# Optimization experiments

Hardware: AMD Instinct MI355X
Metric: run time of the kernel (lower is better)

## Reference

```python
import jax, jax.numpy as jnp
import numpy as np

N = 50000   # nodes (= batch_size = num_e)
D = 256     # d_dim = n_hidden
E = 320000  # edges (first half 'in' direction, second half 'out'/inverse)
R = 400     # relation types (incl. inverses)


def setup_inputs() -> dict:
    key = jax.random.key(0)
    ks = jax.random.split(key, 12)
    s = 0.05  # weight scale so tanh stays in linear-ish range
    w = lambda k, shp: jax.random.normal(k, shp, jnp.float32) * s
    return {
        "emb": jax.random.normal(ks[0], (N, D), jnp.float32),
        "edge_index": jax.random.randint(ks[1], (2, E), 0, N),
        "edge_type": jax.random.randint(ks[2], (E,), 0, R),
        "rel1": w(ks[3], (R, D)),
        "W_in1": w(ks[4], (D, D)),
        "W_out1": w(ks[5], (D, D)),
        "W_loop1": w(ks[6], (D, D)),
        "b1": jnp.zeros((D,), jnp.float32),
        "rel2": w(ks[7], (R, D)),
        "W_in2": w(ks[8], (D, D)),
        "W_out2": w(ks[9], (D, D)),
        "W_loop2": w(ks[10], (D, D)),
        "b2": jnp.zeros((D,), jnp.float32),
        "res": jnp.array([0.1], jnp.float32),
        "mu_w": w(ks[11], (D, D)),
        "mu_b": jnp.zeros((D,), jnp.float32),
        "num_nodes": N,
    }


def _mgcn_conv(x, edge_index, edge_type, rel, W_in, W_out, W_loop, b, n):
    """Relational conv: gather -> compose with relation emb -> direction-split
    linear transform -> degree-normalized scatter-add -> self-loop -> tanh."""
    src, dst = edge_index[0], edge_index[1]
    e = edge_index.shape[1]
    half = e // 2
    m = x[src] * rel[edge_type]                                   # [E, D] compose ('mult')
    m = jnp.concatenate([m[:half] @ W_in, m[half:] @ W_out], 0)    # direction-specific transform
    deg = jax.ops.segment_sum(jnp.ones((e,), x.dtype), dst, num_segments=n)
    norm = 1.0 / jnp.maximum(deg, 1.0)                             # 1/in-degree
    agg = jax.ops.segment_sum(m * norm[dst][:, None], dst, num_segments=n)
    return jnp.tanh(agg + x @ W_loop + b)


def reference(emb, edge_index, edge_type,
              rel1, W_in1, W_out1, W_loop1, b1,
              rel2, W_in2, W_out2, W_loop2, b2,
              res, mu_w, mu_b, num_nodes):
    # forward_base with p.res=True, core_layer=2, dropout in eval mode (identity)
    h = emb + res * _mgcn_conv(emb, edge_index, edge_type, rel1, W_in1, W_out1, W_loop1, b1, num_nodes)
    h = h + res * _mgcn_conv(h, edge_index, edge_type, rel2, W_in2, W_out2, W_loop2, b2, num_nodes)
    # drift head f(t, y) = mu(forward_base(y))
    return h @ mu_w + mu_b
```

## Files before the change

kernel.cpp:

```cpp
#include <hip/hip_runtime.h>
#include <hip/hip_bf16.h>
#include <cstdint>
#include <cstddef>


typedef short bf16x8 __attribute__((ext_vector_type(8)));
typedef float f32x4  __attribute__((ext_vector_type(4)));

__device__ __forceinline__ float b2f(unsigned short u) {
    union { unsigned u32; float f; } c; c.u32 = ((unsigned)u) << 16; return c.f;
}
__device__ __forceinline__ unsigned short f2b(float f) {
    union { float f; unsigned u; } c; c.f = f;
    unsigned r = c.u + 0x7FFFu + ((c.u >> 16) & 1u);
    return (unsigned short)(r >> 16);
}
__device__ __forceinline__ float ftanh(float x) {
    float e = __expf(2.0f * x);
    return 1.0f - __fdividef(2.0f, e + 1.0f);
}

__device__ __forceinline__ unsigned char f2e4m3(float f) {
    unsigned u = __float_as_uint(f);
    unsigned s = (u >> 24) & 0x80u;
    unsigned a = u & 0x7fffffffu;
    if (a >= 0x43e00000u) return (unsigned char)(s | 0x7eu);
    if (a < 0x3c800000u) {
        float m = __uint_as_float(a) * 512.0f;
        int q = (int)rintf(m);
        if (q == 8) return (unsigned char)(s | 0x08u);
        return (unsigned char)(s | (unsigned)q);
    }
    unsigned m = a & 0x7fffffu;
    unsigned e = a >> 23;
    unsigned r = m + 0x7ffffu + ((m >> 20) & 1u);
    if (r >= 0x800000u) { e += 1; r -= 0x800000u; }
    if (e > 127u + 8u) return (unsigned char)(s | 0x7eu);
    return (unsigned char)(s | ((e - 127u + 7u) << 3) | (r >> 20));
}


__global__ void k_hist(const int* __restrict__ dst, int* __restrict__ cnt, int E) {
    int i = blockIdx.x * blockDim.x + threadIdx.x;
    if (i < E) atomicAdd(&cnt[dst[i]], 1);
}

__global__ void k_norm(const int* __restrict__ cnt, float* __restrict__ norm, int N) {
    int i = blockIdx.x * blockDim.x + threadIdx.x;
    if (i < N) norm[i] = 1.0f / fmaxf((float)cnt[i], 1.0f);
}

__global__ void k_scan1(const int* __restrict__ cnt, int* __restrict__ part,
                        int* __restrict__ bsum, int N) {
    __shared__ int s[256];
    int i = blockIdx.x * 256 + threadIdx.x;
    int v = (i < N) ? cnt[i] : 0;
    s[threadIdx.x] = v; __syncthreads();
    #pragma unroll
    for (int o = 1; o < 256; o <<= 1) {
        int t = (threadIdx.x >= o) ? s[threadIdx.x - o] : 0;
        __syncthreads();
        s[threadIdx.x] += t;
        __syncthreads();
    }
    if (i < N) part[i] = s[threadIdx.x] - v;
    if (threadIdx.x == 255) bsum[blockIdx.x] = s[255];
}

__global__ void k_scan2(int* __restrict__ bsum, int nb) {
    __shared__ int s[256];
    int v = (threadIdx.x < nb) ? bsum[threadIdx.x] : 0;
    s[threadIdx.x] = v; __syncthreads();
    #pragma unroll
    for (int o = 1; o < 256; o <<= 1) {
        int t = (threadIdx.x >= o) ? s[threadIdx.x - o] : 0;
        __syncthreads();
        s[threadIdx.x] += t;
        __syncthreads();
    }
    if (threadIdx.x < nb) bsum[threadIdx.x] = s[threadIdx.x] - v;
}

__global__ void k_scan3(const int* __restrict__ part, const int* __restrict__ bsum,
                        int* __restrict__ rowptr, int* __restrict__ cursor, int N, int E) {
    int i = blockIdx.x * 256 + threadIdx.x;
    if (i < N) {
        int r = part[i] + bsum[blockIdx.x];
        rowptr[i] = r; cursor[i] = r;
    }
    if (i == 0) rowptr[N] = E;
}

__global__ void k_scatter(const int* __restrict__ src, const int* __restrict__ dst,
                          const int* __restrict__ et, int* __restrict__ cursor,
                          unsigned* __restrict__ erec, int E, int halfE) {
    int e = blockIdx.x * blockDim.x + threadIdx.x;
    if (e < E) {
        int d = dst[e];
        int pos = atomicAdd(&cursor[d], 1);
        unsigned rec = (unsigned)src[e] | ((unsigned)et[e] << 16)
                     | ((e >= halfE) ? 0x80000000u : 0u);
        erec[pos] = rec;
    }
}


__global__ void k_cvt3(const float* __restrict__ s0, unsigned short* __restrict__ d0, long n0,
                       const float* __restrict__ s1, unsigned short* __restrict__ d1, long n1,
                       const float* __restrict__ s2, unsigned short* __restrict__ d2, long n2) {
    long i = (long)blockIdx.x * blockDim.x + threadIdx.x;
    const float* s; unsigned short* d; long j = i;
    if (j < n0) { s = s0; d = d0; }
    else {
        j -= n0;
        if (j < n1) { s = s1; d = d1; }
        else { j -= n1; if (j >= n2) return; s = s2; d = d2; }
    }
    float4 v = ((const float4*)s)[j];
    ushort4 o;
    o.x = f2b(v.x); o.y = f2b(v.y); o.z = f2b(v.z); o.w = f2b(v.w);
    ((ushort4*)d)[j] = o;
}

__global__ void k_wfrag3(const float* __restrict__ w0, const float* __restrict__ w1,
                         const float* __restrict__ w2, unsigned short* __restrict__ out) {
    int o = blockIdx.x * 256 + threadIdx.x;
    int mi = o >> 16;
    int r  = o & 65535;
    const float* W = (mi == 0) ? w0 : (mi == 1) ? w1 : w2;
    int j  = r & 7;
    int l  = (r >> 3) & 63;
    int nn = (r >> 9) & 15;
    int kg = r >> 13;
    int k = kg * 32 + (l >> 4) * 8 + j;
    int n = nn * 16 + (l & 15);
    out[o] = f2b(W[k * 256 + n]);
}

__global__ void k_wfrag8(const float* __restrict__ w0, const float* __restrict__ w1,
                         const float* __restrict__ w2, const float* __restrict__ w3,
                         unsigned char* __restrict__ out) {
    int o = (blockIdx.x * 256 + threadIdx.x) * 4;
    int mi = o >> 16;
    int r  = o & 65535;
    const float* W = (mi == 0) ? w0 : (mi == 1) ? w1 : (mi == 2) ? w2 : w3;
    int j0 = r & 7;
    int l  = (r >> 3) & 63;
    int nn = (r >> 9) & 15;
    int kg = r >> 13;
    int n  = nn * 16 + (l & 15);
    int kb = kg * 32 + (l >> 4) * 8 + j0;
    unsigned b0 = f2e4m3(W[(kb + 0) * 256 + n]);
    unsigned b1 = f2e4m3(W[(kb + 1) * 256 + n]);
    unsigned b2 = f2e4m3(W[(kb + 2) * 256 + n]);
    unsigned b3 = f2e4m3(W[(kb + 3) * 256 + n]);
    *(unsigned*)(out + o) = b0 | (b1 << 8) | (b2 << 16) | (b3 << 24);
}


__global__ __launch_bounds__(256)
void k_agg(const unsigned short* __restrict__ xb, const unsigned short* __restrict__ relb,
           const int* __restrict__ rowptr, const unsigned* __restrict__ erec,
           const float* __restrict__ norm,
           unsigned char* __restrict__ sIn8, unsigned char* __restrict__ sOut8,
           int N, int D)
{
    const int w = threadIdx.x >> 6, l = threadIdx.x & 63;
    const int v = blockIdx.x * 4 + w;
    if (v >= N) return;
    const int rs = rowptr[v], re = rowptr[v + 1];
    const float nm = norm[v];

    float ai0 = 0, ai1 = 0, ai2 = 0, ai3 = 0;
    float ao0 = 0, ao1 = 0, ao2 = 0, ao3 = 0;

    unsigned c0 = (rs     < re) ? erec[rs]     : 0u;
    unsigned c1 = (rs + 1 < re) ? erec[rs + 1] : 0u;
    unsigned c2 = (rs + 2 < re) ? erec[rs + 2] : 0u;
    unsigned c3 = (rs + 3 < re) ? erec[rs + 3] : 0u;
    int i = rs;
    while (i + 4 <= re) {
        unsigned m0 = (i + 4 < re) ? erec[i + 4] : 0u;
        unsigned m1 = (i + 5 < re) ? erec[i + 5] : 0u;
        unsigned m2 = (i + 6 < re) ? erec[i + 6] : 0u;
        unsigned m3 = (i + 7 < re) ? erec[i + 7] : 0u;
        ushort4 x0 = *(const ushort4*)(xb   + (size_t)(c0 & 0xffff) * D + l * 4);
        ushort4 r0 = *(const ushort4*)(relb + (size_t)((c0 >> 16) & 0x7fff) * D + l * 4);
        ushort4 x1 = *(const ushort4*)(xb   + (size_t)(c1 & 0xffff) * D + l * 4);
        ushort4 r1 = *(const ushort4*)(relb + (size_t)((c1 >> 16) & 0x7fff) * D + l * 4);
        ushort4 x2 = *(const ushort4*)(xb   + (size_t)(c2 & 0xffff) * D + l * 4);
        ushort4 r2 = *(const ushort4*)(relb + (size_t)((c2 >> 16) & 0x7fff) * D + l * 4);
        ushort4 x3 = *(const ushort4*)(xb   + (size_t)(c3 & 0xffff) * D + l * 4);
        ushort4 r3 = *(const ushort4*)(relb + (size_t)((c3 >> 16) & 0x7fff) * D + l * 4);
        float p0, p1, p2, p3;
        p0 = b2f(x0.x)*b2f(r0.x); p1 = b2f(x0.y)*b2f(r0.y);
        p2 = b2f(x0.z)*b2f(r0.z); p3 = b2f(x0.w)*b2f(r0.w);
        if (c0 >> 31) { ao0 += p0; ao1 += p1; ao2 += p2; ao3 += p3; }
        else          { ai0 += p0; ai1 += p1; ai2 += p2; ai3 += p3; }
        p0 = b2f(x1.x)*b2f(r1.x); p1 = b2f(x1.y)*b2f(r1.y);
        p2 = b2f(x1.z)*b2f(r1.z); p3 = b2f(x1.w)*b2f(r1.w);
        if (c1 >> 31) { ao0 += p0; ao1 += p1; ao2 += p2; ao3 += p3; }
        else          { ai0 += p0; ai1 += p1; ai2 += p2; ai3 += p3; }
        p0 = b2f(x2.x)*b2f(r2.x); p1 = b2f(x2.y)*b2f(r2.y);
        p2 = b2f(x2.z)*b2f(r2.z); p3 = b2f(x2.w)*b2f(r2.w);
        if (c2 >> 31) { ao0 += p0; ao1 += p1; ao2 += p2; ao3 += p3; }
        else          { ai0 += p0; ai1 += p1; ai2 += p2; ai3 += p3; }
        p0 = b2f(x3.x)*b2f(r3.x); p1 = b2f(x3.y)*b2f(r3.y);
        p2 = b2f(x3.z)*b2f(r3.z); p3 = b2f(x3.w)*b2f(r3.w);
        if (c3 >> 31) { ao0 += p0; ao1 += p1; ao2 += p2; ao3 += p3; }
        else          { ai0 += p0; ai1 += p1; ai2 += p2; ai3 += p3; }
        c0 = m0; c1 = m1; c2 = m2; c3 = m3; i += 4;
    }
    #pragma unroll
    for (int j = 0; j < 3; ++j) {
        if (i + j < re) {
            unsigned cur = (j == 0) ? c0 : (j == 1) ? c1 : c2;
            ushort4 x0 = *(const ushort4*)(xb   + (size_t)(cur & 0xffff) * D + l * 4);
            ushort4 r0 = *(const ushort4*)(relb + (size_t)((cur >> 16) & 0x7fff) * D + l * 4);
            float p0 = b2f(x0.x)*b2f(r0.x), p1 = b2f(x0.y)*b2f(r0.y);
            float p2 = b2f(x0.z)*b2f(r0.z), p3 = b2f(x0.w)*b2f(r0.w);
            if (cur >> 31) { ao0 += p0; ao1 += p1; ao2 += p2; ao3 += p3; }
            else           { ai0 += p0; ai1 += p1; ai2 += p2; ai3 += p3; }
        }
    }

    unsigned pi = (unsigned)f2e4m3(ai0 * nm)        | ((unsigned)f2e4m3(ai1 * nm) << 8)
                | ((unsigned)f2e4m3(ai2 * nm) << 16) | ((unsigned)f2e4m3(ai3 * nm) << 24);
    unsigned po = (unsigned)f2e4m3(ao0 * nm)        | ((unsigned)f2e4m3(ao1 * nm) << 8)
                | ((unsigned)f2e4m3(ao2 * nm) << 16) | ((unsigned)f2e4m3(ao3 * nm) << 24);
    *(unsigned*)(sIn8  + (size_t)v * 256 + l * 4) = pi;
    *(unsigned*)(sOut8 + (size_t)v * 256 + l * 4) = po;
}


#define FB  do { asm volatile("s_waitcnt lgkmcnt(0)" ::: "memory");             \
                 __builtin_amdgcn_sched_barrier(0);                             \
                 __builtin_amdgcn_s_barrier();                                  \
                 __builtin_amdgcn_sched_barrier(0); } while (0)

#define WRX(AtN, R0, R1) do { *(uint4*)(&(AtN)[wo0]) = R0;                      \
                              *(uint4*)(&(AtN)[wo1]) = R1; } while (0)
#define WR8(AtN, R0)     do { *(uint4*)(((char*)(AtN)) + wf8b) = R0; } while (0)
#define LDX(R0, R1, CB)  do { R0 = *(const uint4*)(a0 + g0 + (CB)*64);          \
                              R1 = *(const uint4*)(a0 + g1 + (CB)*64); } while (0)
#define LD8(R0, SRC, CB) do { R0 = *(const uint4*)((SRC) + gf8 + (CB)*64); } while (0)

#define PBX(Bn, CB)                                                             \
  do { _Pragma("unroll")                                                        \
       for (int kk_ = 0; kk_ < 2; ++kk_) {                                      \
         _Pragma("unroll")                                                      \
         for (int n_ = 0; n_ < 4; ++n_)                                         \
           Bn[kk_*4+n_] = *(const bf16x8*)(WfL +                                \
               ((((CB)*2+kk_)*16 + (w*4+n_))*64 + l)*8);                        \
       } } while (0)

#define PB8(Bn, TBL, CB)                                                        \
  do { _Pragma("unroll")                                                        \
       for (int kk_ = 0; kk_ < 2; ++kk_) {                                      \
         _Pragma("unroll")                                                      \
         for (int n_ = 0; n_ < 4; ++n_)                                         \
           Bn[kk_*4+n_] = *(const long long*)((TBL) +                           \
               ((((CB)*2+kk_)*16 + (w*4+n_))*64 + l)*8);                        \
       } } while (0)

#define MMX(AtC, Bc)                                                            \
  do { _Pragma("unroll")                                                        \
       for (int kk_ = 0; kk_ < 2; ++kk_) {                                      \
         bf16x8 a_[4];                                                          \
         _Pragma("unroll")                                                      \
         for (int m_ = 0; m_ < 4; ++m_) {                                       \
           int rm_ = 16*m_ + lr; int ch_ = (kk_*4+lq) ^ (rm_ & 7);              \
           a_[m_] = *(const bf16x8*)(&(AtC)[rm_*64 + ch_*8]);                   \
         }                                                                      \
         _Pragma("unroll")                                                      \
         for (int m_ = 0; m_ < 4; ++m_) {                                       \
           _Pragma("unroll")                                                    \
           for (int n_ = 0; n_ < 4; ++n_)                                       \
             acc[m_][n_] = __builtin_amdgcn_mfma_f32_16x16x32_bf16(             \
                 a_[m_], Bc[kk_*4+n_], acc[m_][n_], 0, 0, 0);                   \
         } } } while (0)

#define MM8(AtC, Bc)                                                            \
  do { const char* A8_ = (const char*)(AtC);                                    \
       _Pragma("unroll")                                                        \
       for (int kk_ = 0; kk_ < 2; ++kk_) {                                      \
         long long a_[4];                                                       \
         _Pragma("unroll")                                                      \
         for (int m_ = 0; m_ < 4; ++m_) {                                       \
           int rm_ = 16*m_ + lr; int ch_ = (kk_*4+lq) ^ (rm_ & 6);              \
           a_[m_] = *(const long long*)(A8_ + rm_*64 + ch_*8);                  \
         }                                                                      \
         _Pragma("unroll")                                                      \
         for (int m_ = 0; m_ < 4; ++m_) {                                       \
           _Pragma("unroll")                                                    \
           for (int n_ = 0; n_ < 4; ++n_)                                       \
             acc[m_][n_] = __builtin_amdgcn_mfma_f32_16x16x32_fp8_fp8(          \
                 a_[m_], Bc[kk_*4+n_], acc[m_][n_], 0, 0, 0);                   \
         } } } while (0)

template <bool HEAD>
__global__ __launch_bounds__(256, 2)
void k_gemm(const unsigned short* __restrict__ a0,
            const unsigned char*  __restrict__ s8i,
            const unsigned char*  __restrict__ s8o,
            const unsigned short* __restrict__ WfL,
            const unsigned char*  __restrict__ W8I,
            const unsigned char*  __restrict__ W8O,
            const float* __restrict__ bias,
            const float* __restrict__ resPtr,
            const unsigned short* __restrict__ WfMu,
            const float* __restrict__ mub,
            float* __restrict__ outF,
            unsigned short* __restrict__ outB,
            int N, int D)
{
    __shared__ unsigned short lds[HEAD ? 16384 : 8192];
    unsigned short* At0 = lds;
    unsigned short* At1 = lds + 4096;

    const int t = threadIdx.x;
    const int rBase = blockIdx.x * 64;

    const int w  = t >> 6;
    const int l  = t & 63;
    const int lr = l & 15;
    const int lq = l >> 4;

    const int rS0 = t >> 3;
    const int rS1 = rS0 + 32;
    const int cS  = t & 7;
    const int wo0 = rS0 * 64 + ((cS ^ (rS0 & 7)) * 8);
    const int wo1 = rS1 * 64 + ((cS ^ (rS1 & 7)) * 8);
    const size_t g0 = (size_t)min(rBase + rS0, N - 1) * 256 + cS * 8;
    const size_t g1 = (size_t)min(rBase + rS1, N - 1) * 256 + cS * 8;

    const int rf  = t >> 2;
    const int qf  = t & 3;
    const int wf8b = rf * 64 + (((2 * qf) ^ (rf & 6)) * 8);
    const size_t gf8 = (size_t)min(rBase + rf, N - 1) * 256 + qf * 16;

    f32x4 acc[4][4] = {};
    uint4 Ra0, Ra1, Rb0, Rb1, Rc0, Rc1;
    bf16x8 Bb0[8], Bb1[8];
    long long B8a[8], B8b[8];

    LDX(Ra0, Ra1, 0);
    LDX(Rb0, Rb1, 1);
    LDX(Rc0, Rc1, 2);
    PBX(Bb0, 0);
    WRX(At0, Ra0, Ra1);
    FB;

     WRX(At1, Rb0, Rb1); PBX(Bb1, 1);      MMX(At0, Bb0); LDX(Ra0, Ra1, 3); FB;
     WRX(At0, Rc0, Rc1); PBX(Bb0, 2);      MMX(At1, Bb1); LD8(Rb0, s8i, 0); FB;
     WRX(At1, Ra0, Ra1); PBX(Bb1, 3);      MMX(At0, Bb0); LD8(Rc0, s8i, 1); FB;
     WR8(At0, Rb0);      PB8(B8a, W8I, 0); MMX(At1, Bb1); LD8(Ra0, s8i, 2); FB;
     WR8(At1, Rc0);      PB8(B8b, W8I, 1); MM8(At0, B8a); LD8(Rb0, s8i, 3); FB;
     WR8(At0, Ra0);      PB8(B8a, W8I, 2); MM8(At1, B8b); LD8(Rc0, s8o, 0); FB;
     WR8(At1, Rb0);      PB8(B8b, W8I, 3); MM8(At0, B8a); LD8(Ra0, s8o, 1); FB;
     WR8(At0, Rc0);      PB8(B8a, W8O, 0); MM8(At1, B8b); LD8(Rb0, s8o, 2); FB;
     WR8(At1, Ra0);      PB8(B8b, W8O, 1); MM8(At0, B8a); LD8(Rc0, s8o, 3); FB;
     WR8(At0, Rb0);      PB8(B8a, W8O, 2); MM8(At1, B8b); FB;
    WR8(At1, Rc0);      PB8(B8b, W8O, 3); MM8(At0, B8a); FB;
                                          MM8(At1, B8b); FB;

    const int rb4 = lq * 4;
    const float resv = resPtr[0];

    if (!HEAD) {
        unsigned short* C = lds;
        #pragma unroll
        for (int half = 0; half < 2; ++half) {
            if ((w >> 1) == half) {
                #pragma unroll
                for (int m = 0; m < 4; ++m) {
                    #pragma unroll
                    for (int i = 0; i < 4; ++i) {
                        int r6 = 16 * m + rb4 + i;
                        #pragma unroll
                        for (int n = 0; n < 4; ++n) {
                            int cH = (w & 1) * 64 + lr + 16 * n;
                            float v = acc[m][n][i] + bias[half * 128 + cH];
                            C[r6 * 128 + cH] = f2b(resv * ftanh(v));
                        }
                    }
                }
            }
            __syncthreads();
            #pragma unroll
            for (int ii = 0; ii < 4; ++ii) {
                int g   = ii * 256 + t;
                int r   = g >> 4;
                int cc  = g & 15;
                int row = rBase + r;
                if (row < N) {
                    bf16x8 sv = *(const bf16x8*)(&C[r * 128 + cc * 8]);
                    const unsigned short* ar = a0 + (size_t)row * D + half * 128 + cc * 8;
                    uint4 av = *(const uint4*)ar;
                    unsigned aw[4] = { av.x, av.y, av.z, av.w };
                    unsigned ow[4];
                    #pragma unroll
                    for (int p = 0; p < 4; ++p) {
                        float h0 = b2f((unsigned short)(aw[p] & 0xffff)) + b2f((unsigned short)sv[2 * p]);
                        float h1 = b2f((unsigned short)(aw[p] >> 16))    + b2f((unsigned short)sv[2 * p + 1]);
                        ow[p] = (unsigned)f2b(h0) | ((unsigned)f2b(h1) << 16);
                    }
                    *(uint4*)(outB + (size_t)row * D + half * 128 + cc * 8) =
                        make_uint4(ow[0], ow[1], ow[2], ow[3]);
                }
            }
            __syncthreads();
        }
    } else {
        #pragma unroll
        for (int m = 0; m < 4; ++m) {
            #pragma unroll
            for (int i = 0; i < 4; ++i) {
                int row = rBase + 16 * m + rb4 + i;
                if (row < N) {
                    size_t base = (size_t)row * D + w * 64 + lr;
                    int r6 = 16 * m + rb4 + i;
                    #pragma unroll
                    for (int n = 0; n < 4; ++n) {
                        int   c = w * 64 + lr + 16 * n;
                        float v = acc[m][n][i] + bias[c];
                        float h = b2f(a0[base + 16 * n]) + resv * ftanh(v);
                        lds[r6 * 256 + (c ^ ((r6 & 7) << 3))] = f2b(h);
                    }
                }
            }
        }
        __syncthreads();
        #pragma unroll
        for (int m = 0; m < 4; ++m) {
            #pragma unroll
            for (int n = 0; n < 4; ++n)
                acc[m][n] = (f32x4){0.f, 0.f, 0.f, 0.f};
        }

        #pragma unroll
        for (int s2 = 0; s2 < 4; ++s2) {
            #pragma unroll
            for (int kk = 0; kk < 2; ++kk) {
                const int kg = s2 * 2 + kk;
                bf16x8 a_[4], b_[4];
                #pragma unroll
                for (int m = 0; m < 4; ++m) {
                    int rm = 16 * m + lr;
                    int ch = (s2 * 8 + kk * 4 + lq) ^ (rm & 7);
                    a_[m] = *(const bf16x8*)(&lds[rm * 256 + ch * 8]);
                }
                #pragma unroll
                for (int n = 0; n < 4; ++n)
                    b_[n] = *(const bf16x8*)(WfMu + (((kg * 16 + (w * 4 + n)) * 64 + l) * 8));
                #pragma unroll
                for (int m = 0; m < 4; ++m) {
                    #pragma unroll
                    for (int n = 0; n < 4; ++n)
                        acc[m][n] = __builtin_amdgcn_mfma_f32_16x16x32_bf16(a_[m], b_[n], acc[m][n], 0, 0, 0);
                }
            }
        }

        __syncthreads();
        float* Cf = (float*)lds;
        #pragma unroll
        for (int half = 0; half < 2; ++half) {
            if ((w >> 1) == half) {
                #pragma unroll
                for (int m = 0; m < 4; ++m) {
                    #pragma unroll
                    for (int i = 0; i < 4; ++i) {
                        int r6 = 16 * m + rb4 + i;
                        #pragma unroll
                        for (int n = 0; n < 4; ++n) {
                            int cH = (w & 1) * 64 + lr + 16 * n;
                            Cf[r6 * 128 + cH] = acc[m][n][i] + mub[half * 128 + cH];
                        }
                    }
                }
            }
            __syncthreads();
            #pragma unroll
            for (int ii = 0; ii < 8; ++ii) {
                int g   = ii * 256 + t;
                int r   = g >> 5;
                int cc  = g & 31;
                int row = rBase + r;
                if (row < N) {
                    *(float4*)(outF + (size_t)row * D + half * 128 + cc * 4) =
                        *(const float4*)(&Cf[r * 128 + cc * 4]);
                }
            }
            __syncthreads();
        }
    }
}


extern "C" void kernel_launch(void* const* d_in, const int* in_sizes, int n_in,
                              void* d_out, int out_size, void* d_ws, size_t ws_size,
                              hipStream_t stream)
{
    const float* emb  = (const float*)d_in[0];
    const int*   ei   = (const int*)  d_in[1];
    const int*   et   = (const int*)  d_in[2];
    const float* rel1 = (const float*)d_in[3];
    const float* Wi1  = (const float*)d_in[4];
    const float* Wo1  = (const float*)d_in[5];
    const float* Wl1  = (const float*)d_in[6];
    const float* b1   = (const float*)d_in[7];
    const float* rel2 = (const float*)d_in[8];
    const float* Wi2  = (const float*)d_in[9];
    const float* Wo2  = (const float*)d_in[10];
    const float* Wl2  = (const float*)d_in[11];
    const float* b2   = (const float*)d_in[12];
    const float* res  = (const float*)d_in[13];
    const float* muw  = (const float*)d_in[14];
    const float* mub  = (const float*)d_in[15];

    const int D = in_sizes[7];
    const int N = in_sizes[0] / D;
    const int E = in_sizes[2];
    const int R = in_sizes[3] / D;
    const int halfE = E / 2;
    const int* srcA = ei;
    const int* dstA = ei + E;
    const size_t DD = (size_t)D * D;

    char* ws = (char*)d_ws;
    size_t off = 0;
    auto alloc = [&](size_t bytes) -> char* {
        char* p = ws + off; off += (bytes + 255) & ~(size_t)255; return p;
    };
    const int nb1 = (N + 255) / 256;

    float*          norm   = (float*)          alloc((size_t)N * 4);
    int*            cnt    = (int*)            alloc((size_t)N * 4);
    int*            rowptr = (int*)            alloc((size_t)(N + 1) * 4);
    int*            cursor = (int*)            alloc((size_t)N * 4);
    int*            part   = (int*)            alloc((size_t)N * 4);
    int*            bsum   = (int*)            alloc(1024);
    unsigned*       erec   = (unsigned*)       alloc((size_t)E * 4);
    unsigned short* xb     = (unsigned short*) alloc((size_t)N * D * 2);
    unsigned short* h1b    = (unsigned short*) alloc((size_t)N * D * 2);
    unsigned char*  sIn8   = (unsigned char*)  alloc((size_t)N * D);
    unsigned char*  sOut8  = (unsigned char*)  alloc((size_t)N * D);
    unsigned short* r1b    = (unsigned short*) alloc((size_t)R * D * 2);
    unsigned short* r2b    = (unsigned short*) alloc((size_t)R * D * 2);
    unsigned short* fAll   = (unsigned short*) alloc(3 * DD * 2);
    unsigned char*  f8All  = (unsigned char*)  alloc(4 * DD);
    if (off > ws_size) return;

    unsigned short* fWl1 = fAll;
    unsigned short* fWl2 = fAll + DD;
    unsigned short* fMu  = fAll + 2 * DD;
    unsigned char*  f8Wi1 = f8All;
    unsigned char*  f8Wo1 = f8All + DD;
    unsigned char*  f8Wi2 = f8All + 2 * DD;
    unsigned char*  f8Wo2 = f8All + 3 * DD;

    hipMemsetAsync(cnt, 0, (size_t)N * 4, stream);
    k_hist   <<<(E + 255) / 256, 256, 0, stream>>>(dstA, cnt, E);
    k_norm   <<<nb1, 256, 0, stream>>>(cnt, norm, N);
    k_scan1  <<<nb1, 256, 0, stream>>>(cnt, part, bsum, N);
    k_scan2  <<<1,   256, 0, stream>>>(bsum, nb1);
    k_scan3  <<<nb1, 256, 0, stream>>>(part, bsum, rowptr, cursor, N, E);
    k_scatter<<<(E + 255) / 256, 256, 0, stream>>>(srcA, dstA, et, cursor, erec, E, halfE);

    long nd4 = (long)N * D / 4, rd4 = (long)R * D / 4;
    long tot4 = nd4 + 2 * rd4;
    k_cvt3<<<(int)((tot4 + 255) / 256), 256, 0, stream>>>(
        emb, xb, nd4, rel1, r1b, rd4, rel2, r2b, rd4);
    k_wfrag3<<<(int)(3 * DD / 256), 256, 0, stream>>>(Wl1, Wl2, muw, fAll);
    k_wfrag8<<<(int)(4 * DD / 1024), 256, 0, stream>>>(Wi1, Wo1, Wi2, Wo2, f8All);

    const int AB = (N + 3) / 4;
    const int NB = (N + 63) / 64;

    k_agg<<<AB, 256, 0, stream>>>(xb, r1b, rowptr, erec, norm, sIn8, sOut8, N, D);
    k_gemm<false><<<NB, 256, 0, stream>>>(xb, sIn8, sOut8, fWl1, f8Wi1, f8Wo1, b1, res,
                                          nullptr, nullptr, nullptr, h1b, N, D);

    k_agg<<<AB, 256, 0, stream>>>(h1b, r2b, rowptr, erec, norm, sIn8, sOut8, N, D);
    k_gemm<true><<<NB, 256, 0, stream>>>(h1b, sIn8, sOut8, fWl2, f8Wi2, f8Wo2, b2, res,
                                         fMu, mub, (float*)d_out, nullptr, N, D);
}
```

Baseline: 232.5 us.

## Gather node and relation features as FP8 in edge aggregation

After: 206.2 us. 1.13x faster.

```diff
diff --git a/kernel.cpp b/kernel.cpp
--- a/kernel.cpp
+++ b/kernel.cpp
@@ -6,6 +6,7 @@
 
 typedef short bf16x8 __attribute__((ext_vector_type(8)));
 typedef float f32x4  __attribute__((ext_vector_type(4)));
+typedef float f32x2  __attribute__((ext_vector_type(2)));
 
 __device__ __forceinline__ float b2f(unsigned short u) {
     union { unsigned u32; float f; } c; c.u32 = ((unsigned)u) << 16; return c.f;
@@ -37,6 +38,36 @@
     if (r >= 0x800000u) { e += 1; r -= 0x800000u; }
     if (e > 127u + 8u) return (unsigned char)(s | 0x7eu);
     return (unsigned char)(s | ((e - 127u + 7u) << 3) | (r >> 20));
+}
+
+__device__ __forceinline__ unsigned pk8_4(float a, float b, float c, float d) {
+#if __has_builtin(__builtin_amdgcn_cvt_pk_fp8_f32)
+    int v = 0;
+    v = __builtin_amdgcn_cvt_pk_fp8_f32(a, b, v, false);
+    v = __builtin_amdgcn_cvt_pk_fp8_f32(c, d, v, true);
+    return (unsigned)v;
+#else
+    return (unsigned)f2e4m3(a) | ((unsigned)f2e4m3(b) << 8)
+         | ((unsigned)f2e4m3(c) << 16) | ((unsigned)f2e4m3(d) << 24);
+#endif
+}
+
+__device__ __forceinline__ void dec4(unsigned u, float* f) {
+#if __has_builtin(__builtin_amdgcn_cvt_pk_f32_fp8)
+    f32x2 lo = __builtin_amdgcn_cvt_pk_f32_fp8((int)u, false);
+    f32x2 hi = __builtin_amdgcn_cvt_pk_f32_fp8((int)u, true);
+    f[0] = lo[0]; f[1] = lo[1]; f[2] = hi[0]; f[3] = hi[1];
+#else
+    #pragma unroll
+    for (int i = 0; i < 4; ++i) {
+        unsigned b = (u >> (8 * i)) & 0xffu;
+        unsigned em = b & 0x7fu;
+        float mag;
+        if (em >= 8u) mag = __uint_as_float((((em >> 3) + 120u) << 23) | ((em & 7u) << 20));
+        else          mag = (float)em * 0.001953125f;
+        f[i] = (b & 0x80u) ? -mag : mag;
+    }
+#endif
 }
 
 
@@ -105,21 +136,25 @@
 }
 
 
-__global__ void k_cvt3(const float* __restrict__ s0, unsigned short* __restrict__ d0, long n0,
-                       const float* __restrict__ s1, unsigned short* __restrict__ d1, long n1,
-                       const float* __restrict__ s2, unsigned short* __restrict__ d2, long n2) {
+__global__ void k_cvtx3(const float* __restrict__ s0, unsigned short* __restrict__ d0,
+                        unsigned char* __restrict__ e0, long n0,
+                        const float* __restrict__ s1, unsigned short* __restrict__ d1,
+                        unsigned char* __restrict__ e1, long n1,
+                        const float* __restrict__ s2, unsigned short* __restrict__ d2,
+                        unsigned char* __restrict__ e2, long n2) {
     long i = (long)blockIdx.x * blockDim.x + threadIdx.x;
-    const float* s; unsigned short* d; long j = i;
-    if (j < n0) { s = s0; d = d0; }
+    const float* s; unsigned short* d; unsigned char* e; long j = i;
+    if (j < n0) { s = s0; d = d0; e = e0; }
     else {
         j -= n0;
-        if (j < n1) { s = s1; d = d1; }
-        else { j -= n1; if (j >= n2) return; s = s2; d = d2; }
+        if (j < n1) { s = s1; d = d1; e = e1; }
+        else { j -= n1; if (j >= n2) return; s = s2; d = d2; e = e2; }
     }
     float4 v = ((const float4*)s)[j];
     ushort4 o;
     o.x = f2b(v.x); o.y = f2b(v.y); o.z = f2b(v.z); o.w = f2b(v.w);
     ((ushort4*)d)[j] = o;
+    ((unsigned*)e)[j] = pk8_4(v.x, v.y, v.z, v.w);
 }
 
 __global__ void k_wfrag3(const float* __restrict__ w0, const float* __restrict__ w1,
@@ -150,16 +185,13 @@
     int kg = r >> 13;
     int n  = nn * 16 + (l & 15);
     int kb = kg * 32 + (l >> 4) * 8 + j0;
-    unsigned b0 = f2e4m3(W[(kb + 0) * 256 + n]);
-    unsigned b1 = f2e4m3(W[(kb + 1) * 256 + n]);
-    unsigned b2 = f2e4m3(W[(kb + 2) * 256 + n]);
-    unsigned b3 = f2e4m3(W[(kb + 3) * 256 + n]);
-    *(unsigned*)(out + o) = b0 | (b1 << 8) | (b2 << 16) | (b3 << 24);
+    *(unsigned*)(out + o) = pk8_4(W[(kb + 0) * 256 + n], W[(kb + 1) * 256 + n],
+                                  W[(kb + 2) * 256 + n], W[(kb + 3) * 256 + n]);
 }
 
 
 __global__ __launch_bounds__(256)
-void k_agg(const unsigned short* __restrict__ xb, const unsigned short* __restrict__ relb,
+void k_agg(const unsigned char* __restrict__ x8, const unsigned char* __restrict__ rel8,
            const int* __restrict__ rowptr, const unsigned* __restrict__ erec,
            const float* __restrict__ norm,
            unsigned char* __restrict__ sIn8, unsigned char* __restrict__ sOut8,
@@ -184,52 +216,44 @@
         unsigned m1 = (i + 5 < re) ? erec[i + 5] : 0u;
         unsigned m2 = (i + 6 < re) ? erec[i + 6] : 0u;
         unsigned m3 = (i + 7 < re) ? erec[i + 7] : 0u;
-        ushort4 x0 = *(const ushort4*)(xb   + (size_t)(c0 & 0xffff) * D + l * 4);
-        ushort4 r0 = *(const ushort4*)(relb + (size_t)((c0 >> 16) & 0x7fff) * D + l * 4);
-        ushort4 x1 = *(const ushort4*)(xb   + (size_t)(c1 & 0xffff) * D + l * 4);
-        ushort4 r1 = *(const ushort4*)(relb + (size_t)((c1 >> 16) & 0x7fff) * D + l * 4);
-        ushort4 x2 = *(const ushort4*)(xb   + (size_t)(c2 & 0xffff) * D + l * 4);
-        ushort4 r2 = *(const ushort4*)(relb + (size_t)((c2 >> 16) & 0x7fff) * D + l * 4);
-        ushort4 x3 = *(const ushort4*)(xb   + (size_t)(c3 & 0xffff) * D + l * 4);
-        ushort4 r3 = *(const ushort4*)(relb + (size_t)((c3 >> 16) & 0x7fff) * D + l * 4);
-        float p0, p1, p2, p3;
-        p0 = b2f(x0.x)*b2f(r0.x); p1 = b2f(x0.y)*b2f(r0.y);
-        p2 = b2f(x0.z)*b2f(r0.z); p3 = b2f(x0.w)*b2f(r0.w);
-        if (c0 >> 31) { ao0 += p0; ao1 += p1; ao2 += p2; ao3 += p3; }
-        else          { ai0 += p0; ai1 += p1; ai2 += p2; ai3 += p3; }
-        p0 = b2f(x1.x)*b2f(r1.x); p1 = b2f(x1.y)*b2f(r1.y);
-        p2 = b2f(x1.z)*b2f(r1.z); p3 = b2f(x1.w)*b2f(r1.w);
-        if (c1 >> 31) { ao0 += p0; ao1 += p1; ao2 += p2; ao3 += p3; }
-        else          { ai0 += p0; ai1 += p1; ai2 += p2; ai3 += p3; }
-        p0 = b2f(x2.x)*b2f(r2.x); p1 = b2f(x2.y)*b2f(r2.y);
-        p2 = b2f(x2.z)*b2f(r2.z); p3 = b2f(x2.w)*b2f(r2.w);
-        if (c2 >> 31) { ao0 += p0; ao1 += p1; ao2 += p2; ao3 += p3; }
-        else          { ai0 += p0; ai1 += p1; ai2 += p2; ai3 += p3; }
-        p0 = b2f(x3.x)*b2f(r3.x); p1 = b2f(x3.y)*b2f(r3.y);
-        p2 = b2f(x3.z)*b2f(r3.z); p3 = b2f(x3.w)*b2f(r3.w);
-        if (c3 >> 31) { ao0 += p0; ao1 += p1; ao2 += p2; ao3 += p3; }
-        else          { ai0 += p0; ai1 += p1; ai2 += p2; ai3 += p3; }
+        unsigned xu0 = *(const unsigned*)(x8   + (size_t)(c0 & 0xffff) * 256 + l * 4);
+        unsigned ru0 = *(const unsigned*)(rel8 + (size_t)((c0 >> 16) & 0x7fff) * 256 + l * 4);
+        unsigned xu1 = *(const unsigned*)(x8   + (size_t)(c1 & 0xffff) * 256 + l * 4);
+        unsigned ru1 = *(const unsigned*)(rel8 + (size_t)((c1 >> 16) & 0x7fff) * 256 + l * 4);
+        unsigned xu2 = *(const unsigned*)(x8   + (size_t)(c2 & 0xffff) * 256 + l * 4);
+        unsigned ru2 = *(const unsigned*)(rel8 + (size_t)((c2 >> 16) & 0x7fff) * 256 + l * 4);
+        unsigned xu3 = *(const unsigned*)(x8   + (size_t)(c3 & 0xffff) * 256 + l * 4);
+        unsigned ru3 = *(const unsigned*)(rel8 + (size_t)((c3 >> 16) & 0x7fff) * 256 + l * 4);
+        float xf[4], rf[4];
+        dec4(xu0, xf); dec4(ru0, rf);
+        if (c0 >> 31) { ao0 += xf[0]*rf[0]; ao1 += xf[1]*rf[1]; ao2 += xf[2]*rf[2]; ao3 += xf[3]*rf[3]; }
+        else          { ai0 += xf[0]*rf[0]; ai1 += xf[1]*rf[1]; ai2 += xf[2]*rf[2]; ai3 += xf[3]*rf[3]; }
+        dec4(xu1, xf); dec4(ru1, rf);
+        if (c1 >> 31) { ao0 += xf[0]*rf[0]; ao1 += xf[1]*rf[1]; ao2 += xf[2]*rf[2]; ao3 += xf[3]*rf[3]; }
+        else          { ai0 += xf[0]*rf[0]; ai1 += xf[1]*rf[1]; ai2 += xf[2]*rf[2]; ai3 += xf[3]*rf[3]; }
+        dec4(xu2, xf); dec4(ru2, rf);
+        if (c2 >> 31) { ao0 += xf[0]*rf[0]; ao1 += xf[1]*rf[1]; ao2 += xf[2]*rf[2]; ao3 += xf[3]*rf[3]; }
+        else          { ai0 += xf[0]*rf[0]; ai1 += xf[1]*rf[1]; ai2 += xf[2]*rf[2]; ai3 += xf[3]*rf[3]; }
+        dec4(xu3, xf); dec4(ru3, rf);
+        if (c3 >> 31) { ao0 += xf[0]*rf[0]; ao1 += xf[1]*rf[1]; ao2 += xf[2]*rf[2]; ao3 += xf[3]*rf[3]; }
+        else          { ai0 += xf[0]*rf[0]; ai1 += xf[1]*rf[1]; ai2 += xf[2]*rf[2]; ai3 += xf[3]*rf[3]; }
         c0 = m0; c1 = m1; c2 = m2; c3 = m3; i += 4;
     }
     #pragma unroll
     for (int j = 0; j < 3; ++j) {
         if (i + j < re) {
             unsigned cur = (j == 0) ? c0 : (j == 1) ? c1 : c2;
-            ushort4 x0 = *(const ushort4*)(xb   + (size_t)(cur & 0xffff) * D + l * 4);
-            ushort4 r0 = *(const ushort4*)(relb + (size_t)((cur >> 16) & 0x7fff) * D + l * 4);
-            float p0 = b2f(x0.x)*b2f(r0.x), p1 = b2f(x0.y)*b2f(r0.y);
-            float p2 = b2f(x0.z)*b2f(r0.z), p3 = b2f(x0.w)*b2f(r0.w);
-            if (cur >> 31) { ao0 += p0; ao1 += p1; ao2 += p2; ao3 += p3; }
-            else           { ai0 += p0; ai1 += p1; ai2 += p2; ai3 += p3; }
+            unsigned xu = *(const unsigned*)(x8   + (size_t)(cur & 0xffff) * 256 + l * 4);
+            unsigned ru = *(const unsigned*)(rel8 + (size_t)((cur >> 16) & 0x7fff) * 256 + l * 4);
+            float xf[4], rf[4];
+            dec4(xu, xf); dec4(ru, rf);
+            if (cur >> 31) { ao0 += xf[0]*rf[0]; ao1 += xf[1]*rf[1]; ao2 += xf[2]*rf[2]; ao3 += xf[3]*rf[3]; }
+            else           { ai0 += xf[0]*rf[0]; ai1 += xf[1]*rf[1]; ai2 += xf[2]*rf[2]; ai3 += xf[3]*rf[3]; }
         }
     }
 
-    unsigned pi = (unsigned)f2e4m3(ai0 * nm)        | ((unsigned)f2e4m3(ai1 * nm) << 8)
-                | ((unsigned)f2e4m3(ai2 * nm) << 16) | ((unsigned)f2e4m3(ai3 * nm) << 24);
-    unsigned po = (unsigned)f2e4m3(ao0 * nm)        | ((unsigned)f2e4m3(ao1 * nm) << 8)
-                | ((unsigned)f2e4m3(ao2 * nm) << 16) | ((unsigned)f2e4m3(ao3 * nm) << 24);
-    *(unsigned*)(sIn8  + (size_t)v * 256 + l * 4) = pi;
-    *(unsigned*)(sOut8 + (size_t)v * 256 + l * 4) = po;
+    *(unsigned*)(sIn8  + (size_t)v * 256 + l * 4) = pk8_4(ai0 * nm, ai1 * nm, ai2 * nm, ai3 * nm);
+    *(unsigned*)(sOut8 + (size_t)v * 256 + l * 4) = pk8_4(ao0 * nm, ao1 * nm, ao2 * nm, ao3 * nm);
 }
 
 
@@ -312,6 +336,7 @@
             const float* __restrict__ mub,
             float* __restrict__ outF,
             unsigned short* __restrict__ outB,
+            unsigned char* __restrict__ outB8,
             int N, int D)
 {
     __shared__ unsigned short lds[HEAD ? 16384 : 8192];
@@ -399,14 +424,20 @@
                     uint4 av = *(const uint4*)ar;
                     unsigned aw[4] = { av.x, av.y, av.z, av.w };
                     unsigned ow[4];
+                    float hv[8];
                     #pragma unroll
                     for (int p = 0; p < 4; ++p) {
                         float h0 = b2f((unsigned short)(aw[p] & 0xffff)) + b2f((unsigned short)sv[2 * p]);
                         float h1 = b2f((unsigned short)(aw[p] >> 16))    + b2f((unsigned short)sv[2 * p + 1]);
+                        hv[2 * p] = h0; hv[2 * p + 1] = h1;
                         ow[p] = (unsigned)f2b(h0) | ((unsigned)f2b(h1) << 16);
                     }
                     *(uint4*)(outB + (size_t)row * D + half * 128 + cc * 8) =
                         make_uint4(ow[0], ow[1], ow[2], ow[3]);
+                    uint2 q;
+                    q.x = pk8_4(hv[0], hv[1], hv[2], hv[3]);
+                    q.y = pk8_4(hv[4], hv[5], hv[6], hv[7]);
+                    *(uint2*)(outB8 + (size_t)row * 256 + half * 128 + cc * 8) = q;
                 }
             }
             __syncthreads();
@@ -544,10 +575,14 @@
     unsigned*       erec   = (unsigned*)       alloc((size_t)E * 4);
     unsigned short* xb     = (unsigned short*) alloc((size_t)N * D * 2);
     unsigned short* h1b    = (unsigned short*) alloc((size_t)N * D * 2);
+    unsigned char*  x8     = (unsigned char*)  alloc((size_t)N * D);
+    unsigned char*  h18    = (unsigned char*)  alloc((size_t)N * D);
     unsigned char*  sIn8   = (unsigned char*)  alloc((size_t)N * D);
     unsigned char*  sOut8  = (unsigned char*)  alloc((size_t)N * D);
     unsigned short* r1b    = (unsigned short*) alloc((size_t)R * D * 2);
     unsigned short* r2b    = (unsigned short*) alloc((size_t)R * D * 2);
+    unsigned char*  r18    = (unsigned char*)  alloc((size_t)R * D);
+    unsigned char*  r28    = (unsigned char*)  alloc((size_t)R * D);
     unsigned short* fAll   = (unsigned short*) alloc(3 * DD * 2);
     unsigned char*  f8All  = (unsigned char*)  alloc(4 * DD);
     if (off > ws_size) return;
@@ -570,19 +605,19 @@
 
     long nd4 = (long)N * D / 4, rd4 = (long)R * D / 4;
     long tot4 = nd4 + 2 * rd4;
-    k_cvt3<<<(int)((tot4 + 255) / 256), 256, 0, stream>>>(
-        emb, xb, nd4, rel1, r1b, rd4, rel2, r2b, rd4);
+    k_cvtx3<<<(int)((tot4 + 255) / 256), 256, 0, stream>>>(
+        emb, xb, x8, nd4, rel1, r1b, r18, rd4, rel2, r2b, r28, rd4);
     k_wfrag3<<<(int)(3 * DD / 256), 256, 0, stream>>>(Wl1, Wl2, muw, fAll);
     k_wfrag8<<<(int)(4 * DD / 1024), 256, 0, stream>>>(Wi1, Wo1, Wi2, Wo2, f8All);
 
     const int AB = (N + 3) / 4;
     const int NB = (N + 63) / 64;
 
-    k_agg<<<AB, 256, 0, stream>>>(xb, r1b, rowptr, erec, norm, sIn8, sOut8, N, D);
+    k_agg<<<AB, 256, 0, stream>>>(x8, r18, rowptr, erec, norm, sIn8, sOut8, N, D);
     k_gemm<false><<<NB, 256, 0, stream>>>(xb, sIn8, sOut8, fWl1, f8Wi1, f8Wo1, b1, res,
-                                          nullptr, nullptr, nullptr, h1b, N, D);
-
-    k_agg<<<AB, 256, 0, stream>>>(h1b, r2b, rowptr, erec, norm, sIn8, sOut8, N, D);
+                                          nullptr, nullptr, nullptr, h1b, h18, N, D);
+
+    k_agg<<<AB, 256, 0, stream>>>(h18, r28, rowptr, erec, norm, sIn8, sOut8, N, D);
     k_gemm<true><<<NB, 256, 0, stream>>>(h1b, sIn8, sOut8, fWl2, f8Wi2, f8Wo2, b2, res,
-                                         fMu, mub, (float*)d_out, nullptr, N, D);
-}
+                                         fMu, mub, (float*)d_out, nullptr, nullptr, N, D);
+}
```
